# Kernel tuning notes

Hardware: AMD Instinct MI355X
Metric: run time of the kernel (lower is better)

The kernel has to match this reference:

```python
import jax, jax.numpy as jnp
import numpy as np

N_EMBD = 768
N_HEAD = 12
DIM_HEAD = N_EMBD // N_HEAD


def setup_inputs() -> dict:
    key = jax.random.key(0)
    k1, k2, k3 = jax.random.split(key, 3)
    B, T = 4, 2048
    x = jax.random.normal(k1, (B, T, N_EMBD), dtype=jnp.float32)
    # torch Linear(n_embd, 3*n_embd, bias=False): y = x @ W.T, W:[3C,C].
    # Store pre-transposed [C,3C] for direct matmul.
    s = 1.0 / np.sqrt(N_EMBD)
    W_qkv = jax.random.uniform(k2, (N_EMBD, 3 * N_EMBD), dtype=jnp.float32, minval=-s, maxval=s)
    W_proj = jax.random.uniform(k3, (N_EMBD, N_EMBD), dtype=jnp.float32, minval=-s, maxval=s)
    return {"x": x, "W_qkv": W_qkv, "W_proj": W_proj}


def reference(x, W_qkv, W_proj):
    B, T, C = x.shape
    qkv = x @ W_qkv                                  # [B,T,3C]
    q, k, v = jnp.split(qkv, 3, axis=-1)
    def heads(t):  # [B,T,C] -> [B,H,T,Dh]
        return t.reshape(B, T, N_HEAD, DIM_HEAD).transpose(0, 2, 1, 3)
    q, k, v = heads(q), heads(k), heads(v)
    # Source divides by scale = dim_head**-0.5, i.e. multiplies by sqrt(dim_head).
    scores = jnp.einsum('bhtd,bhsd->bhts', q, k) * jnp.sqrt(jnp.float32(DIM_HEAD))
    attn = jax.nn.softmax(scores, axis=-1)           # [B,H,T,T] materialized
    y = jnp.einsum('bhts,bhsd->bhtd', attn, v)       # [B,H,T,Dh]
    y = y.transpose(0, 2, 1, 3).reshape(B, T, C)
    return y @ W_proj
```

## Files before the change

kernel.cpp:

```cpp
#include <hip/hip_runtime.h>

typedef _Float16 f16;
typedef f16 f16x4 __attribute__((ext_vector_type(4)));
typedef f16 f16x8 __attribute__((ext_vector_type(8)));
typedef __fp16 h16x2 __attribute__((ext_vector_type(2)));
typedef float floatx4 __attribute__((ext_vector_type(4)));

#define LDT 72
#define LDTV 136
#define QSCALE 11.5415603271117f

__global__ __launch_bounds__(256) void convert_f32_f16(const float* __restrict__ in,
                                                       f16* __restrict__ out, int n) {
  int i = (blockIdx.x * 256 + threadIdx.x) * 4;
  if (i >= n) return;
  float4 v = *(const float4*)(in + i);
  f16x4 o = {(f16)v.x, (f16)v.y, (f16)v.z, (f16)v.w};
  *(f16x4*)(out + i) = o;
}

__global__ __launch_bounds__(256) void transpose_f32_f16_tiled(const float* __restrict__ in,
                                                               f16* __restrict__ out,
                                                               int K, int N) {
  __shared__ f16 tile[64][LDT];
  int k0 = blockIdx.x * 64, n0 = blockIdx.y * 64;
  int tid = threadIdx.x;
  int r = tid >> 4, c4 = (tid & 15) * 4;
  for (int p = 0; p < 4; ++p) {
    int rr = r + p * 16;
    float4 v = *(const float4*)(in + (size_t)(k0 + rr) * N + n0 + c4);
    tile[c4 + 0][rr] = (f16)v.x;
    tile[c4 + 1][rr] = (f16)v.y;
    tile[c4 + 2][rr] = (f16)v.z;
    tile[c4 + 3][rr] = (f16)v.w;
  }
  __syncthreads();
  int rn = tid >> 3, ck = (tid & 7) * 8;
  for (int p = 0; p < 2; ++p) {
    int rr = rn + p * 32;
    *(uint4*)(out + (size_t)(n0 + rr) * K + k0 + ck) = *(const uint4*)(&tile[rr][ck]);
  }
}

__global__ __launch_bounds__(256) void gemm1_qkv(const f16* __restrict__ A,
                                                 const f16* __restrict__ Bt,
                                                 f16* __restrict__ q16, f16* __restrict__ k16,
                                                 f16* __restrict__ vt) {
  __shared__ f16 As[128 * LDT];
  __shared__ f16 Bs[128 * LDT];
  int tid = threadIdx.x;
  int lane = tid & 63, wid = tid >> 6;
  int quad = lane >> 4, l16 = lane & 15;
  int wy = wid >> 1, wx = wid & 1;
  int m0 = blockIdx.x * 128, n0 = blockIdx.y * 128;
  int srow = tid >> 3, scol = (tid & 7) * 8;
  floatx4 acc[4][4] = {};
  for (int k0 = 0; k0 < 768; k0 += 64) {
    for (int p = 0; p < 4; ++p) {
      int r = srow + p * 32;
      *(uint4*)(As + r * LDT + scol) = *(const uint4*)(A + (size_t)(m0 + r) * 768 + k0 + scol);
      *(uint4*)(Bs + r * LDT + scol) = *(const uint4*)(Bt + (size_t)(n0 + r) * 768 + k0 + scol);
    }
    __syncthreads();
    for (int kk = 0; kk < 64; kk += 32) {
      f16x8 af[4], bfr[4];
      for (int i = 0; i < 4; ++i)
        af[i] = *(const f16x8*)(As + (wy * 64 + i * 16 + l16) * LDT + kk + quad * 8);
      for (int j = 0; j < 4; ++j)
        bfr[j] = *(const f16x8*)(Bs + (wx * 64 + j * 16 + l16) * LDT + kk + quad * 8);
      for (int i = 0; i < 4; ++i)
        for (int j = 0; j < 4; ++j)
          acc[i][j] = __builtin_amdgcn_mfma_f32_16x16x32_f16(af[i], bfr[j], acc[i][j], 0, 0, 0);
    }
    __syncthreads();
  }
  for (int i = 0; i < 4; ++i)
    for (int j = 0; j < 4; ++j)
      for (int r = 0; r < 4; ++r) {
        int row = m0 + wy * 64 + i * 16 + quad * 4 + r;
        int col = n0 + wx * 64 + j * 16 + l16;
        float a = acc[i][j][r];
        int b = row >> 11, t = row & 2047;
        if (col < 768) {
          int h = col >> 6, d = col & 63;
          q16[((size_t)(b * 12 + h)) * 131072 + (size_t)t * 64 + d] = (f16)(a * QSCALE);
        } else if (col < 1536) {
          int c = col - 768;
          int h = c >> 6, d = c & 63;
          k16[((size_t)(b * 12 + h)) * 131072 + (size_t)t * 64 + d] = (f16)a;
        } else {
          int c = col - 1536;
          int h = c >> 6, d = c & 63;
          vt[((size_t)(b * 12 + h)) * 131072 + (size_t)d * 2048 + t] = (f16)a;
        }
      }
}

__global__ __launch_bounds__(256) void gemm_bt_f16(const f16* __restrict__ A,
                                                   const f16* __restrict__ Bt,
                                                   float* __restrict__ C,
                                                   int M, int N, int K) {
  __shared__ f16 As[128 * LDT];
  __shared__ f16 Bs[128 * LDT];
  int tid = threadIdx.x;
  int lane = tid & 63, wid = tid >> 6;
  int quad = lane >> 4, l16 = lane & 15;
  int wy = wid >> 1, wx = wid & 1;
  int m0 = blockIdx.x * 128, n0 = blockIdx.y * 128;
  int srow = tid >> 3, scol = (tid & 7) * 8;
  floatx4 acc[4][4] = {};
  for (int k0 = 0; k0 < K; k0 += 64) {
    for (int p = 0; p < 4; ++p) {
      int r = srow + p * 32;
      *(uint4*)(As + r * LDT + scol) = *(const uint4*)(A + (size_t)(m0 + r) * K + k0 + scol);
      *(uint4*)(Bs + r * LDT + scol) = *(const uint4*)(Bt + (size_t)(n0 + r) * K + k0 + scol);
    }
    __syncthreads();
    for (int kk = 0; kk < 64; kk += 32) {
      f16x8 af[4], bfr[4];
      for (int i = 0; i < 4; ++i)
        af[i] = *(const f16x8*)(As + (wy * 64 + i * 16 + l16) * LDT + kk + quad * 8);
      for (int j = 0; j < 4; ++j)
        bfr[j] = *(const f16x8*)(Bs + (wx * 64 + j * 16 + l16) * LDT + kk + quad * 8);
      for (int i = 0; i < 4; ++i)
        for (int j = 0; j < 4; ++j)
          acc[i][j] = __builtin_amdgcn_mfma_f32_16x16x32_f16(af[i], bfr[j], acc[i][j], 0, 0, 0);
    }
    __syncthreads();
  }
  for (int i = 0; i < 4; ++i) {
    int row = m0 + wy * 64 + i * 16 + quad * 4;
    for (int j = 0; j < 4; ++j) {
      int col = n0 + wx * 64 + j * 16 + l16;
      for (int r = 0; r < 4; ++r)
        C[(size_t)(row + r) * N + col] = acc[i][j][r];
    }
  }
}

__global__ __launch_bounds__(256, 2) void flash_attn(const f16* __restrict__ q16,
                                                     const f16* __restrict__ k16,
                                                     const f16* __restrict__ vT,
                                                     f16* __restrict__ y) {
  __shared__ f16 Ks[128 * LDT];
  __shared__ f16 Vt[64 * LDTV];
  const int T = 2048;
  int xcd = blockIdx.x & 7, yb = blockIdx.x >> 3;
  int bh = xcd * 6 + (yb >> 5);
  int qt = yb & 31;
  int b = bh / 12, h = bh - b * 12;
  int tid = threadIdx.x;
  int lane = tid & 63, wid = tid >> 6;
  int quad = lane >> 4, l16 = lane & 15;
  int rk = tid >> 3, ck = (tid & 7) * 8;
  int rv = tid >> 4, cv = (tid & 15) * 8;
  size_t hb = (size_t)bh * T * 64;

  f16x8 qf[2];
  {
    size_t qrow = hb + (size_t)(qt * 64 + wid * 16 + l16) * 64 + quad * 8;
    qf[0] = *(const f16x8*)(q16 + qrow);
    qf[1] = *(const f16x8*)(q16 + qrow + 32);
  }
  f16x4 ones4;
  for (int e = 0; e < 4; ++e) ones4[e] = (f16)1.0f;

  float m_i = -1e30f, l_i = 0.f;
  floatx4 o[4] = {};

  for (int kt = 0; kt < 16; ++kt) {
    if (kt) __syncthreads();
    for (int p = 0; p < 4; ++p) {
      int r = rk + p * 32;
      *(uint4*)(Ks + r * LDT + ck) =
          *(const uint4*)(k16 + hb + (size_t)(kt * 128 + r) * 64 + ck);
      int d = rv + p * 16;
      *(uint4*)(Vt + d * LDTV + cv) =
          *(const uint4*)(vT + hb + (size_t)d * T + kt * 128 + cv);
    }
    __syncthreads();

    floatx4 sf[8];
    const floatx4 z4 = {0.f, 0.f, 0.f, 0.f};
    for (int i = 0; i < 8; ++i) sf[i] = z4;
    for (int kk = 0; kk < 2; ++kk)
      for (int i = 0; i < 8; ++i) {
        f16x8 kf = *(const f16x8*)(Ks + (i * 16 + l16) * LDT + kk * 32 + quad * 8);
        sf[i] = __builtin_amdgcn_mfma_f32_16x16x32_f16(kf, qf[kk], sf[i], 0, 0, 0);
      }

    float mx = fmaxf(fmaxf(sf[0][0], sf[0][1]), fmaxf(sf[0][2], sf[0][3]));
    for (int i = 1; i < 8; ++i)
      mx = fmaxf(mx, fmaxf(fmaxf(sf[i][0], sf[i][1]), fmaxf(sf[i][2], sf[i][3])));
    mx = fmaxf(mx, __shfl_xor(mx, 16));
    mx = fmaxf(mx, __shfl_xor(mx, 32));
    float m_new = fmaxf(m_i, mx);
    float alpha = exp2f(m_i - m_new);
    m_i = m_new;
    for (int i = 0; i < 8; ++i)
      for (int r = 0; r < 4; ++r) sf[i][r] = exp2f(sf[i][r] - m_new);
    for (int i = 0; i < 4; ++i) o[i] *= alpha;

    f16x4 pf[8];
    for (int i = 0; i < 8; ++i) {
      union { h16x2 h; f16 f[2]; } lo, hi;
      lo.h = __builtin_amdgcn_cvt_pkrtz(sf[i][0], sf[i][1]);
      hi.h = __builtin_amdgcn_cvt_pkrtz(sf[i][2], sf[i][3]);
      pf[i][0] = lo.f[0]; pf[i][1] = lo.f[1];
      pf[i][2] = hi.f[0]; pf[i][3] = hi.f[1];
    }

    floatx4 rs = z4;
    for (int si = 0; si < 8; ++si)
      rs = __builtin_amdgcn_mfma_f32_16x16x16f16(ones4, pf[si], rs, 0, 0, 0);
    l_i = l_i * alpha + rs[0];

    for (int i = 0; i < 4; ++i)
      for (int si = 0; si < 8; ++si) {
        f16x4 vf = *(const f16x4*)(Vt + (i * 16 + l16) * LDTV + si * 16 + quad * 4);
        o[i] = __builtin_amdgcn_mfma_f32_16x16x16f16(vf, pf[si], o[i], 0, 0, 0);
      }
  }

  float invl = 1.0f / l_i;
  int t = qt * 64 + wid * 16 + l16;
  size_t off = ((size_t)(b * T + t)) * 768 + h * 64;
  for (int i = 0; i < 4; ++i)
    for (int r = 0; r < 4; ++r)
      y[off + i * 16 + quad * 4 + r] = (f16)(o[i][r] * invl);
}

extern "C" void kernel_launch(void* const* d_in, const int* in_sizes, int n_in,
                              void* d_out, int out_size, void* d_ws, size_t ws_size,
                              hipStream_t stream) {
  const float* x     = (const float*)d_in[0];
  const float* Wqkv  = (const float*)d_in[1];
  const float* Wproj = (const float*)d_in[2];
  float* out = (float*)d_out;
  char* ws = (char*)d_ws;
  f16* x16    = (f16*)ws;
  f16* q16    = (f16*)(ws + 12582912);
  f16* k16    = (f16*)(ws + 25165824);
  f16* vT16   = (f16*)(ws + 37748736);
  f16* y16    = (f16*)(ws + 50331648);
  f16* WqkvT  = (f16*)(ws + 62914560);
  f16* WprojT = (f16*)(ws + 66453504);

  convert_f32_f16<<<6144, 256, 0, stream>>>(x, x16, 6291456);
  transpose_f32_f16_tiled<<<dim3(12, 36), 256, 0, stream>>>(Wqkv, WqkvT, 768, 2304);
  transpose_f32_f16_tiled<<<dim3(12, 12), 256, 0, stream>>>(Wproj, WprojT, 768, 768);
  gemm1_qkv<<<dim3(64, 18), 256, 0, stream>>>(x16, WqkvT, q16, k16, vT16);
  flash_attn<<<1536, 256, 0, stream>>>(q16, k16, vT16, y16);
  gemm_bt_f16<<<dim3(64, 6), 256, 0, stream>>>(y16, WprojT, out, 8192, 768, 768);
}
```

Before: 275.1 us.

## Fuse x conversion into QKV GEMM, enlarge attention blocks, swizzle LDS, use f16 exp2

```diff
diff --git a/kernel.cpp b/kernel.cpp
--- a/kernel.cpp
+++ b/kernel.cpp
@@ -7,17 +7,7 @@
 typedef float floatx4 __attribute__((ext_vector_type(4)));
 
 #define LDT 72
-#define LDTV 136
 #define QSCALE 11.5415603271117f
-
-__global__ __launch_bounds__(256) void convert_f32_f16(const float* __restrict__ in,
-                                                       f16* __restrict__ out, int n) {
-  int i = (blockIdx.x * 256 + threadIdx.x) * 4;
-  if (i >= n) return;
-  float4 v = *(const float4*)(in + i);
-  f16x4 o = {(f16)v.x, (f16)v.y, (f16)v.z, (f16)v.w};
-  *(f16x4*)(out + i) = o;
-}
 
 __global__ __launch_bounds__(256) void transpose_f32_f16_tiled(const float* __restrict__ in,
                                                                f16* __restrict__ out,
@@ -42,7 +32,7 @@
   }
 }
 
-__global__ __launch_bounds__(256) void gemm1_qkv(const f16* __restrict__ A,
+__global__ __launch_bounds__(256) void gemm1_qkv(const float* __restrict__ A,
                                                  const f16* __restrict__ Bt,
                                                  f16* __restrict__ q16, f16* __restrict__ k16,
                                                  f16* __restrict__ vt) {
@@ -58,7 +48,12 @@
   for (int k0 = 0; k0 < 768; k0 += 64) {
     for (int p = 0; p < 4; ++p) {
       int r = srow + p * 32;
-      *(uint4*)(As + r * LDT + scol) = *(const uint4*)(A + (size_t)(m0 + r) * 768 + k0 + scol);
+      const float* src = A + (size_t)(m0 + r) * 768 + k0 + scol;
+      float4 v0 = *(const float4*)(src);
+      float4 v1 = *(const float4*)(src + 4);
+      f16x8 hv = {(f16)v0.x, (f16)v0.y, (f16)v0.z, (f16)v0.w,
+                  (f16)v1.x, (f16)v1.y, (f16)v1.z, (f16)v1.w};
+      *(f16x8*)(As + r * LDT + scol) = hv;
       *(uint4*)(Bs + r * LDT + scol) = *(const uint4*)(Bt + (size_t)(n0 + r) * 768 + k0 + scol);
     }
     __syncthreads();
@@ -138,27 +133,29 @@
   }
 }
 
-__global__ __launch_bounds__(256, 2) void flash_attn(const f16* __restrict__ q16,
+__global__ __launch_bounds__(512, 1) void flash_attn(const f16* __restrict__ q16,
                                                      const f16* __restrict__ k16,
                                                      const f16* __restrict__ vT,
                                                      f16* __restrict__ y) {
-  __shared__ f16 Ks[128 * LDT];
-  __shared__ f16 Vt[64 * LDTV];
+  __shared__ f16 Ks[128 * 64];
+  __shared__ f16 Vt[64 * 128];
   const int T = 2048;
   int xcd = blockIdx.x & 7, yb = blockIdx.x >> 3;
-  int bh = xcd * 6 + (yb >> 5);
-  int qt = yb & 31;
+  int bh = xcd * 6 + (yb >> 4);
+  int qt = yb & 15;
   int b = bh / 12, h = bh - b * 12;
   int tid = threadIdx.x;
   int lane = tid & 63, wid = tid >> 6;
   int quad = lane >> 4, l16 = lane & 15;
-  int rk = tid >> 3, ck = (tid & 7) * 8;
-  int rv = tid >> 4, cv = (tid & 15) * 8;
+  int rk = tid >> 3, kch = tid & 7;
+  int rv = tid >> 4, vch = tid & 15;
+  int kswz = (kch ^ (rk & 7)) * 8;
+  int vswz = (vch ^ (rv & 15)) * 8;
   size_t hb = (size_t)bh * T * 64;
 
   f16x8 qf[2];
   {
-    size_t qrow = hb + (size_t)(qt * 64 + wid * 16 + l16) * 64 + quad * 8;
+    size_t qrow = hb + (size_t)(qt * 128 + wid * 16 + l16) * 64 + quad * 8;
     qf[0] = *(const f16x8*)(q16 + qrow);
     qf[1] = *(const f16x8*)(q16 + qrow + 32);
   }
@@ -170,13 +167,13 @@
 
   for (int kt = 0; kt < 16; ++kt) {
     if (kt) __syncthreads();
-    for (int p = 0; p < 4; ++p) {
-      int r = rk + p * 32;
-      *(uint4*)(Ks + r * LDT + ck) =
-          *(const uint4*)(k16 + hb + (size_t)(kt * 128 + r) * 64 + ck);
-      int d = rv + p * 16;
-      *(uint4*)(Vt + d * LDTV + cv) =
-          *(const uint4*)(vT + hb + (size_t)d * T + kt * 128 + cv);
+    for (int p = 0; p < 2; ++p) {
+      int r = rk + p * 64;
+      *(uint4*)(Ks + r * 64 + kswz) =
+          *(const uint4*)(k16 + hb + (size_t)(kt * 128 + r) * 64 + kch * 8);
+      int d = rv + p * 32;
+      *(uint4*)(Vt + d * 128 + vswz) =
+          *(const uint4*)(vT + hb + (size_t)d * T + kt * 128 + vch * 8);
     }
     __syncthreads();
 
@@ -185,7 +182,8 @@
     for (int i = 0; i < 8; ++i) sf[i] = z4;
     for (int kk = 0; kk < 2; ++kk)
       for (int i = 0; i < 8; ++i) {
-        f16x8 kf = *(const f16x8*)(Ks + (i * 16 + l16) * LDT + kk * 32 + quad * 8);
+        int row = i * 16 + l16;
+        f16x8 kf = *(const f16x8*)(Ks + row * 64 + (((kk * 4 + quad) ^ (l16 & 7)) * 8));
         sf[i] = __builtin_amdgcn_mfma_f32_16x16x32_f16(kf, qf[kk], sf[i], 0, 0, 0);
       }
 
@@ -197,17 +195,19 @@
     float m_new = fmaxf(m_i, mx);
     float alpha = exp2f(m_i - m_new);
     m_i = m_new;
-    for (int i = 0; i < 8; ++i)
-      for (int r = 0; r < 4; ++r) sf[i][r] = exp2f(sf[i][r] - m_new);
     for (int i = 0; i < 4; ++i) o[i] *= alpha;
 
     f16x4 pf[8];
     for (int i = 0; i < 8; ++i) {
-      union { h16x2 h; f16 f[2]; } lo, hi;
-      lo.h = __builtin_amdgcn_cvt_pkrtz(sf[i][0], sf[i][1]);
-      hi.h = __builtin_amdgcn_cvt_pkrtz(sf[i][2], sf[i][3]);
-      pf[i][0] = lo.f[0]; pf[i][1] = lo.f[1];
-      pf[i][2] = hi.f[0]; pf[i][3] = hi.f[1];
+      union { h16x2 h; f16 f[2]; } a2, b2;
+      a2.h = __builtin_amdgcn_cvt_pkrtz(sf[i][0] - m_new, sf[i][1] - m_new);
+      b2.h = __builtin_amdgcn_cvt_pkrtz(sf[i][2] - m_new, sf[i][3] - m_new);
+      f16x4 uu = {a2.f[0], a2.f[1], b2.f[0], b2.f[1]};
+#if __has_builtin(__builtin_elementwise_exp2)
+      pf[i] = __builtin_elementwise_exp2(uu);
+#else
+      for (int r = 0; r < 4; ++r) pf[i][r] = (f16)exp2f((float)uu[r]);
+#endif
     }
 
     floatx4 rs = z4;
@@ -217,13 +217,15 @@
 
     for (int i = 0; i < 4; ++i)
       for (int si = 0; si < 8; ++si) {
-        f16x4 vf = *(const f16x4*)(Vt + (i * 16 + l16) * LDTV + si * 16 + quad * 4);
+        int d = i * 16 + l16;
+        int cch = si * 2 + (quad >> 1);
+        f16x4 vf = *(const f16x4*)(Vt + d * 128 + ((cch ^ l16) * 8) + (quad & 1) * 4);
         o[i] = __builtin_amdgcn_mfma_f32_16x16x16f16(vf, pf[si], o[i], 0, 0, 0);
       }
   }
 
   float invl = 1.0f / l_i;
-  int t = qt * 64 + wid * 16 + l16;
+  int t = qt * 128 + wid * 16 + l16;
   size_t off = ((size_t)(b * T + t)) * 768 + h * 64;
   for (int i = 0; i < 4; ++i)
     for (int r = 0; r < 4; ++r)
@@ -238,18 +240,16 @@
   const float* Wproj = (const float*)d_in[2];
   float* out = (float*)d_out;
   char* ws = (char*)d_ws;
-  f16* x16    = (f16*)ws;
-  f16* q16    = (f16*)(ws + 12582912);
-  f16* k16    = (f16*)(ws + 25165824);
-  f16* vT16   = (f16*)(ws + 37748736);
-  f16* y16    = (f16*)(ws + 50331648);
-  f16* WqkvT  = (f16*)(ws + 62914560);
-  f16* WprojT = (f16*)(ws + 66453504);
-
-  convert_f32_f16<<<6144, 256, 0, stream>>>(x, x16, 6291456);
+  f16* q16    = (f16*)ws;
+  f16* k16    = (f16*)(ws + 12582912);
+  f16* vT16   = (f16*)(ws + 25165824);
+  f16* y16    = (f16*)(ws + 37748736);
+  f16* WqkvT  = (f16*)(ws + 50331648);
+  f16* WprojT = (f16*)(ws + 53870592);
+
   transpose_f32_f16_tiled<<<dim3(12, 36), 256, 0, stream>>>(Wqkv, WqkvT, 768, 2304);
   transpose_f32_f16_tiled<<<dim3(12, 12), 256, 0, stream>>>(Wproj, WprojT, 768, 768);
-  gemm1_qkv<<<dim3(64, 18), 256, 0, stream>>>(x16, WqkvT, q16, k16, vT16);
-  flash_attn<<<1536, 256, 0, stream>>>(q16, k16, vT16, y16);
+  gemm1_qkv<<<dim3(64, 18), 256, 0, stream>>>(x, WqkvT, q16, k16, vT16);
+  flash_attn<<<768, 512, 0, stream>>>(q16, k16, vT16, y16);
   gemm_bt_f16<<<dim3(64, 6), 256, 0, stream>>>(y16, WprojT, out, 8192, 768, 768);
 }
```

After: 259.4 us. -5.7%, faster.
